# Performance work log

Measured on AMD Instinct MI355X. Metric: run time of the kernel, lower is better.

The kernel has to match this reference:

```python
import jax, jax.numpy as jnp
import numpy as np

N_HEADS = 8
D_MODEL = 128
EPS = 1e-6


def setup_inputs() -> dict:
    key = jax.random.key(0)
    k1, k2, k3, k4, k5 = jax.random.split(key, 5)
    B, Dim, F, T = 1, D_MODEL, 256, 1024
    queries = jax.random.normal(k1, (B, Dim, F, T), dtype=jnp.float32)
    keys = jax.random.normal(k2, (B, Dim, F, T), dtype=jnp.float32)
    values = jax.random.normal(k3, (B, Dim, F, T), dtype=jnp.float32)
    # out_projection: Linear(d_model, d_output) with d_output == d_model
    W_out = jax.random.normal(k4, (D_MODEL, D_MODEL), dtype=jnp.float32) / np.sqrt(D_MODEL)
    b_out = jax.random.normal(k5, (D_MODEL,), dtype=jnp.float32) * 0.01
    return {"queries": queries, "keys": keys, "values": values,
            "W_out": W_out, "b_out": b_out}


def _to_heads(x, B, Dim, L, H):
    # (B, Dim, F, T) -> (B, L, Dim) -> (B, L, H, d) -> (B, H, L, d)
    return x.reshape(B, Dim, L).transpose(0, 2, 1).reshape(B, L, H, Dim // H).transpose(0, 2, 1, 3)


def reference(queries, keys, values, W_out, b_out):
    B, Dim, F, T = queries.shape
    L = F * T
    H = N_HEADS
    q = jax.nn.sigmoid(_to_heads(queries, B, Dim, L, H))  # (B,H,L,d)
    k = jax.nn.sigmoid(_to_heads(keys, B, Dim, L, H))
    v = _to_heads(values, B, Dim, L, H)

    # NOTE: sums are over the HEAD axis (dim=1), faithful to the original code
    ks = k.sum(axis=1, keepdims=True)                      # (B,1,L,d)
    qs = q.sum(axis=1, keepdims=True)
    sink_incoming = 1.0 / jnp.sum((q + EPS) * (ks + EPS), axis=-1)      # (B,H,L)
    source_outgoing = 1.0 / jnp.sum((k + EPS) * (qs + EPS), axis=-1)    # (B,H,L)
    conserved_sink = jnp.sum(
        (q + EPS) * ((k * source_outgoing[..., None]).sum(axis=1, keepdims=True) + EPS),
        axis=-1)                                                        # (B,H,L)
    conserved_source = jnp.sum(
        (k + EPS) * ((q * sink_incoming[..., None]).sum(axis=1, keepdims=True) + EPS),
        axis=-1)
    conserved_source = jnp.clip(conserved_source, -1.0, 1.0)
    sink_allocation = jax.nn.sigmoid(conserved_sink * (float(L) / float(L)))
    source_competition = jax.nn.softmax(conserved_source, axis=-1) * float(L)

    kv = jnp.einsum('bhld,bhlm->bhdm', k, v * source_competition[..., None])
    qkv = jnp.einsum('bhld,bhdm->bhlm', q * sink_incoming[..., None], kv)
    x = (qkv * sink_allocation[..., None]).transpose(0, 2, 1, 3).reshape(B, L, Dim)
    x = x @ W_out.T + b_out                                 # dropout is identity (eval)
    return x.transpose(0, 2, 1).reshape(B, Dim, F, T)
```

## Files before the change

kernel.cpp:

```cpp
#include <hip/hip_runtime.h>
#include <hip/hip_bf16.h>

#define L_TOT (1 << 18)
#define L_SHIFT 18
#define NHEAD 8
#define DHEAD 16
#define DMODEL 128
#define EPSF 1e-6f

typedef float f32x4 __attribute__((ext_vector_type(4)));
typedef short bf16x8 __attribute__((ext_vector_type(8)));

__device__ __forceinline__ float frcp(float x) { return __builtin_amdgcn_rcpf(x); }
__device__ __forceinline__ float sigm(float x) { return frcp(1.0f + __expf(-x)); }
__device__ __forceinline__ unsigned short f2bf(float f) {
    return (unsigned short)((__float_as_uint(f) + 0x8000u) >> 16);
}

__device__ __forceinline__ float qsum(float x) {
    x += __int_as_float(__builtin_amdgcn_update_dpp(0, __float_as_int(x), 0xB1, 0xf, 0xf, true));
    x += __int_as_float(__builtin_amdgcn_update_dpp(0, __float_as_int(x), 0x4E, 0xf, 0xf, true));
    return x;
}

__global__ __launch_bounds__(256) void k1_stats(
        const float* __restrict__ Q, const float* __restrict__ K,
        float* __restrict__ scale_o, float* __restrict__ wbuf,
        float* __restrict__ sep) {
    __shared__ float hredl[4][8];

    const int t = threadIdx.x;
    const int l0 = blockIdx.x * 64;
    const int c = t >> 2;
    const int s = t & 3;
    const int l = l0 + c;

    float qv[32], kv[32];
#pragma unroll
    for (int h = 0; h < 8; ++h)
#pragma unroll
        for (int r = 0; r < 4; ++r) {
            const int p = h * 16 + s * 4 + r;
            qv[h * 4 + r] = Q[(p << L_SHIFT) + l];
            kv[h * 4 + r] = K[(p << L_SHIFT) + l];
        }

    unsigned a[32];
#pragma unroll
    for (int i = 0; i < 32; ++i) {
        const unsigned qu = __float_as_uint(sigm(qv[i])) + 0x8000u;
        const unsigned ku = __float_as_uint(sigm(kv[i])) + 0x8000u;
        a[i] = __builtin_amdgcn_perm(ku, qu, 0x07060302u);
    }

    float ks[4] = {0.f, 0.f, 0.f, 0.f}, qs[4] = {0.f, 0.f, 0.f, 0.f};
#pragma unroll
    for (int h = 0; h < 8; ++h)
#pragma unroll
        for (int j = 0; j < 4; ++j) {
            const unsigned u = a[h * 4 + j];
            qs[j] += __uint_as_float(u << 16);
            ks[j] += __uint_as_float(u & 0xffff0000u);
        }

    float kse[4], qse[4];
#pragma unroll
    for (int j = 0; j < 4; ++j) { kse[j] = ks[j] + EPSF; qse[j] = qs[j] + EPSF; }

    float si[8], so[8];
#pragma unroll
    for (int h = 0; h < 8; ++h) {
        float aq = 0.f, ak = 0.f;
#pragma unroll
        for (int j = 0; j < 4; ++j) {
            const unsigned u = a[h * 4 + j];
            aq += __uint_as_float(u << 16) * kse[j];
            ak += __uint_as_float(u & 0xffff0000u) * qse[j];
        }
        si[h] = frcp(qsum(aq));
        so[h] = frcp(qsum(ak));
    }

    float kso[4] = {0.f, 0.f, 0.f, 0.f}, qsi[4] = {0.f, 0.f, 0.f, 0.f};
#pragma unroll
    for (int h = 0; h < 8; ++h)
#pragma unroll
        for (int j = 0; j < 4; ++j) {
            const unsigned u = a[h * 4 + j];
            kso[j] += __uint_as_float(u & 0xffff0000u) * so[h];
            qsi[j] += __uint_as_float(u << 16) * si[h];
        }
#pragma unroll
    for (int j = 0; j < 4; ++j) { kse[j] = kso[j] + EPSF; qse[j] = qsi[j] + EPSF; }

    float e2[2], sc2[2];
#pragma unroll
    for (int h = 0; h < 8; ++h) {
        float aq = 0.f, ak = 0.f;
#pragma unroll
        for (int j = 0; j < 4; ++j) {
            const unsigned u = a[h * 4 + j];
            aq += __uint_as_float(u << 16) * kse[j];
            ak += __uint_as_float(u & 0xffff0000u) * qse[j];
        }
        const float ck = qsum(aq);
        float cs = qsum(ak);
        if ((h >> 1) == s) {
            cs = fminf(fmaxf(cs, -1.f), 1.f);
            e2[h & 1] = __expf(cs);
            sc2[h & 1] = sigm(ck) * si[h];
        }
    }

    wbuf[((2 * s + 0) << L_SHIFT) + l] = e2[0];
    wbuf[((2 * s + 1) << L_SHIFT) + l] = e2[1];
    scale_o[((2 * s + 0) << L_SHIFT) + l] = sc2[0];
    scale_o[((2 * s + 1) << L_SHIFT) + l] = sc2[1];

    float v0 = e2[0], v1 = e2[1];
    v0 += __shfl_xor(v0, 4, 64);  v1 += __shfl_xor(v1, 4, 64);
    v0 += __shfl_xor(v0, 8, 64);  v1 += __shfl_xor(v1, 8, 64);
    v0 += __shfl_xor(v0, 16, 64); v1 += __shfl_xor(v1, 16, 64);
    v0 += __shfl_xor(v0, 32, 64); v1 += __shfl_xor(v1, 32, 64);
    if ((t & 63) < 4) {
        const int w = t >> 6;
        hredl[w][2 * s + 0] = v0;
        hredl[w][2 * s + 1] = v1;
    }
    __syncthreads();
    if (t < 8)
        sep[blockIdx.x * 8 + t] = hredl[0][t] + hredl[1][t] + hredl[2][t] + hredl[3][t];
}

__global__ __launch_bounds__(256) void k2_kv(
        const float* __restrict__ Kg, const float* __restrict__ Vg,
        const float* __restrict__ wg, float* __restrict__ parts) {
    __shared__ float kvred[4][256];
    const int b = blockIdx.x;
    const int h = b >> 7;
    const int blk = b & 127;
    const int t = threadIdx.x;
    const int wv = t >> 6, lane = t & 63;
    const int lq = lane & 15, lh = lane >> 4;

    const int rowKV = ((h * DHEAD + lq) << L_SHIFT);
    const int rowW  = (h << L_SHIFT);
    const int lbase = blk * 2048 + wv * 512 + lh * 8;

    f32x4 acc = {0.f, 0.f, 0.f, 0.f};
#pragma unroll 4
    for (int ch = 0; ch < 16; ++ch) {
        const int lo = lbase + ch * 32;
        const float4 ka = *(const float4*)&Kg[rowKV + lo];
        const float4 kb = *(const float4*)&Kg[rowKV + lo + 4];
        const float4 va = *(const float4*)&Vg[rowKV + lo];
        const float4 vb = *(const float4*)&Vg[rowKV + lo + 4];
        const float4 wa = *(const float4*)&wg[rowW + lo];
        const float4 wb = *(const float4*)&wg[rowW + lo + 4];
        bf16x8 af, bvf;
        af[0] = (short)f2bf(sigm(ka.x) * wa.x);
        af[1] = (short)f2bf(sigm(ka.y) * wa.y);
        af[2] = (short)f2bf(sigm(ka.z) * wa.z);
        af[3] = (short)f2bf(sigm(ka.w) * wa.w);
        af[4] = (short)f2bf(sigm(kb.x) * wb.x);
        af[5] = (short)f2bf(sigm(kb.y) * wb.y);
        af[6] = (short)f2bf(sigm(kb.z) * wb.z);
        af[7] = (short)f2bf(sigm(kb.w) * wb.w);
        bvf[0] = (short)f2bf(va.x);
        bvf[1] = (short)f2bf(va.y);
        bvf[2] = (short)f2bf(va.z);
        bvf[3] = (short)f2bf(va.w);
        bvf[4] = (short)f2bf(vb.x);
        bvf[5] = (short)f2bf(vb.y);
        bvf[6] = (short)f2bf(vb.z);
        bvf[7] = (short)f2bf(vb.w);
        acc = __builtin_amdgcn_mfma_f32_16x16x32_bf16(af, bvf, acc, 0, 0, 0);
    }

#pragma unroll
    for (int r = 0; r < 4; ++r)
        kvred[wv][(lh * 4 + r) * 16 + lq] = acc[r];
    __syncthreads();
    parts[b * 256 + t] = kvred[0][t] + kvred[1][t] + kvred[2][t] + kvred[3][t];
}

__global__ __launch_bounds__(256) void k3_wkv(
        const float* __restrict__ Wg, const float* __restrict__ parts,
        const float* __restrict__ sep, unsigned* __restrict__ wkvb) {
    const int hb = blockIdx.x;
    const int t = threadIdx.x;
    __shared__ float kvf[256];
    __shared__ float redl[4];

    float p = 0.f;
#pragma unroll
    for (int i = 0; i < 16; ++i) p += sep[(t + i * 256) * 8 + hb];
#pragma unroll
    for (int o = 32; o >= 1; o >>= 1) p += __shfl_xor(p, o, 64);
    if ((t & 63) == 0) redl[t >> 6] = p;

    float kacc = 0.f;
    for (int j = 0; j < 128; ++j)
        kacc += parts[(hb * 128 + j) * 256 + t];

    __syncthreads();
    const float s = (float)L_TOT / (redl[0] + redl[1] + redl[2] + redl[3]);
    kvf[t] = kacc * s;
    __syncthreads();

#pragma unroll
    for (int i = 0; i < 4; ++i) {
        const int j = t + i * 256;
        const int dim = j & 127, prp = j >> 7;
        float a0 = 0.f, a1 = 0.f;
#pragma unroll
        for (int mm = 0; mm < 16; ++mm) {
            const float wv = Wg[dim * 128 + hb * 16 + mm];
            a0 += wv * kvf[(2 * prp) * 16 + mm];
            a1 += wv * kvf[(2 * prp + 1) * 16 + mm];
        }
        wkvb[dim * 64 + hb * 8 + prp] = ((unsigned)f2bf(a1) << 16) | f2bf(a0);
    }
}

__global__ __launch_bounds__(256) void k4_mfma(
        const float* __restrict__ Q, const float* __restrict__ scale_g,
        const unsigned* __restrict__ wkvb, const float* __restrict__ bg,
        float* __restrict__ out) {
    __shared__ unsigned A_lds[128 * 68];
    __shared__ float bias[128];
    const int t = threadIdx.x;

#pragma unroll
    for (int i = 0; i < 8; ++i) {
        const int idx4 = t + i * 256;
        const uint4 v = ((const uint4*)wkvb)[idx4];
        const int row = idx4 >> 4, c4 = idx4 & 15;
        *(uint4*)&A_lds[row * 68 + c4 * 4] = v;
    }
    if (t < 128) bias[t] = bg[t];
    __syncthreads();

    const int w = t >> 6, lane = t & 63;
    const int lq = lane & 15, lh = lane >> 4;

#pragma unroll
    for (int ci = 0; ci < 2; ++ci) {
        const int l = blockIdx.x * 128 + ci * 64 + w * 16 + lq;

        float qv[4][8];
        float scv[4];
#pragma unroll
        for (int ks = 0; ks < 4; ++ks) {
            scv[ks] = scale_g[((ks * 2 + (lane >> 5)) << L_SHIFT) + l];
#pragma unroll
            for (int j = 0; j < 8; ++j) {
                const int p = ks * 32 + lh * 8 + j;
                qv[ks][j] = Q[(p << L_SHIFT) + l];
            }
        }
        bf16x8 bfr[4];
#pragma unroll
        for (int ks = 0; ks < 4; ++ks)
#pragma unroll
            for (int j = 0; j < 8; ++j)
                bfr[ks][j] = (short)f2bf(sigm(qv[ks][j]) * scv[ks]);

        f32x4 acc[8];
#pragma unroll
        for (int mt = 0; mt < 8; ++mt)
            acc[mt] = *(const f32x4*)&bias[mt * 16 + lh * 4];

#pragma unroll
        for (int ks = 0; ks < 4; ++ks) {
#pragma unroll
            for (int mt = 0; mt < 8; ++mt) {
                const int row = mt * 16 + lq;
                const bf16x8 aA = *(const bf16x8*)&A_lds[row * 68 + ks * 16 + lh * 4];
                acc[mt] = __builtin_amdgcn_mfma_f32_16x16x32_bf16(aA, bfr[ks], acc[mt], 0, 0, 0);
            }
        }

#pragma unroll
        for (int mt = 0; mt < 8; ++mt) {
#pragma unroll
            for (int r = 0; r < 4; ++r) {
                const int dim = mt * 16 + lh * 4 + r;
                out[(dim << L_SHIFT) + l] = acc[mt][r];
            }
        }
    }
}

extern "C" void kernel_launch(void* const* d_in, const int* in_sizes, int n_in,
                              void* d_out, int out_size, void* d_ws, size_t ws_size,
                              hipStream_t stream) {
    const float* Q = (const float*)d_in[0];
    const float* K = (const float*)d_in[1];
    const float* V = (const float*)d_in[2];
    const float* W = (const float*)d_in[3];
    const float* B = (const float*)d_in[4];
    float* out = (float*)d_out;
    float* ws = (float*)d_ws;

    float* parts    = ws;
    unsigned* wkvb  = (unsigned*)(ws + 262144);
    float* sep      = ws + 270336;
    float* scale    = ws + 303104;
    float* wbuf     = scale + 8 * L_TOT;

    k1_stats<<<L_TOT / 64, 256, 0, stream>>>(Q, K, scale, wbuf, sep);
    k2_kv<<<NHEAD * 128, 256, 0, stream>>>(K, V, wbuf, parts);
    k3_wkv<<<NHEAD, 256, 0, stream>>>(W, parts, sep, wkvb);
    k4_mfma<<<L_TOT / 128, 256, 0, stream>>>(Q, scale, wkvb, B, out);
}
```

Baseline: 190.6 us.

## Process four column groups per k1 block with software-pipelined loads

k1_stats now handles 256 positions per block instead of 64, looping over four 64-column chunks. The next chunk's Q/K loads are issued before the current chunk's stats are computed, so memory latency overlaps with compute. Per-block exp partial sums are accumulated across chunks, so the sep buffer shrinks and k3's reduction loop over it is cut to match. The cost is higher register pressure (two 32-element load buffers plus the packed array) and a quarter as many blocks, which may reduce occupancy and latency hiding.

```diff
diff --git a/kernel.cpp b/kernel.cpp
--- a/kernel.cpp
+++ b/kernel.cpp
@@ -23,36 +23,32 @@
     return x;
 }
 
-__global__ __launch_bounds__(256) void k1_stats(
+__device__ __forceinline__ void k1_load(
         const float* __restrict__ Q, const float* __restrict__ K,
-        float* __restrict__ scale_o, float* __restrict__ wbuf,
-        float* __restrict__ sep) {
-    __shared__ float hredl[4][8];
-
-    const int t = threadIdx.x;
-    const int l0 = blockIdx.x * 64;
-    const int c = t >> 2;
-    const int s = t & 3;
-    const int l = l0 + c;
-
-    float qv[32], kv[32];
+        int l, int s, float* qv, float* kvv) {
 #pragma unroll
     for (int h = 0; h < 8; ++h)
 #pragma unroll
         for (int r = 0; r < 4; ++r) {
             const int p = h * 16 + s * 4 + r;
-            qv[h * 4 + r] = Q[(p << L_SHIFT) + l];
-            kv[h * 4 + r] = K[(p << L_SHIFT) + l];
-        }
-
-    unsigned a[32];
+            qv[h * 4 + r]  = Q[(p << L_SHIFT) + l];
+            kvv[h * 4 + r] = K[(p << L_SHIFT) + l];
+        }
+}
+
+__device__ __forceinline__ void k1_pack(const float* qv, const float* kvv, unsigned* a) {
 #pragma unroll
     for (int i = 0; i < 32; ++i) {
         const unsigned qu = __float_as_uint(sigm(qv[i])) + 0x8000u;
-        const unsigned ku = __float_as_uint(sigm(kv[i])) + 0x8000u;
+        const unsigned ku = __float_as_uint(sigm(kvv[i])) + 0x8000u;
         a[i] = __builtin_amdgcn_perm(ku, qu, 0x07060302u);
     }
-
+}
+
+__device__ __forceinline__ void k1_body(
+        const unsigned* a, int l, int s,
+        float* __restrict__ scale_o, float* __restrict__ wbuf,
+        float& acc0, float& acc1) {
     float ks[4] = {0.f, 0.f, 0.f, 0.f}, qs[4] = {0.f, 0.f, 0.f, 0.f};
 #pragma unroll
     for (int h = 0; h < 8; ++h)
@@ -117,7 +113,40 @@
     scale_o[((2 * s + 0) << L_SHIFT) + l] = sc2[0];
     scale_o[((2 * s + 1) << L_SHIFT) + l] = sc2[1];
 
-    float v0 = e2[0], v1 = e2[1];
+    acc0 += e2[0];
+    acc1 += e2[1];
+}
+
+__global__ __launch_bounds__(256) void k1_stats(
+        const float* __restrict__ Q, const float* __restrict__ K,
+        float* __restrict__ scale_o, float* __restrict__ wbuf,
+        float* __restrict__ sep) {
+    __shared__ float hredl[4][8];
+
+    const int t = threadIdx.x;
+    const int s = t & 3;
+    const int cq = t >> 2;
+    const int lb = blockIdx.x * 256 + cq;
+
+    float qv[32], kvv[32];
+    unsigned a[32];
+    float acc0 = 0.f, acc1 = 0.f;
+
+    k1_load(Q, K, lb, s, qv, kvv);
+
+    k1_pack(qv, kvv, a);
+    k1_load(Q, K, lb + 64, s, qv, kvv);
+    k1_body(a, lb, s, scale_o, wbuf, acc0, acc1);
+    k1_pack(qv, kvv, a);
+    k1_load(Q, K, lb + 128, s, qv, kvv);
+    k1_body(a, lb + 64, s, scale_o, wbuf, acc0, acc1);
+    k1_pack(qv, kvv, a);
+    k1_load(Q, K, lb + 192, s, qv, kvv);
+    k1_body(a, lb + 128, s, scale_o, wbuf, acc0, acc1);
+    k1_pack(qv, kvv, a);
+    k1_body(a, lb + 192, s, scale_o, wbuf, acc0, acc1);
+
+    float v0 = acc0, v1 = acc1;
     v0 += __shfl_xor(v0, 4, 64);  v1 += __shfl_xor(v1, 4, 64);
     v0 += __shfl_xor(v0, 8, 64);  v1 += __shfl_xor(v1, 8, 64);
     v0 += __shfl_xor(v0, 16, 64); v1 += __shfl_xor(v1, 16, 64);
@@ -194,7 +223,7 @@
 
     float p = 0.f;
 #pragma unroll
-    for (int i = 0; i < 16; ++i) p += sep[(t + i * 256) * 8 + hb];
+    for (int i = 0; i < 4; ++i) p += sep[(t + i * 256) * 8 + hb];
 #pragma unroll
     for (int o = 32; o >= 1; o >>= 1) p += __shfl_xor(p, o, 64);
     if ((t & 63) == 0) redl[t >> 6] = p;
@@ -309,7 +338,7 @@
     float* scale    = ws + 303104;
     float* wbuf     = scale + 8 * L_TOT;
 
-    k1_stats<<<L_TOT / 64, 256, 0, stream>>>(Q, K, scale, wbuf, sep);
+    k1_stats<<<L_TOT / 256, 256, 0, stream>>>(Q, K, scale, wbuf, sep);
     k2_kv<<<NHEAD * 128, 256, 0, stream>>>(K, V, wbuf, parts);
     k3_wkv<<<NHEAD, 256, 0, stream>>>(W, parts, sep, wkvb);
     k4_mfma<<<L_TOT / 128, 256, 0, stream>>>(Q, scale, wkvb, B, out);
```

Result: slower. 200.5 us (+5.2%).

## Fuse stats and KV-accumulation kernels so sigmoid weights stay in LDS

Applied to the files above, without the earlier changes.

Merges the per-position stats kernel and the K^T·V MFMA accumulation kernel into one kernel. Each block processes 256 positions in four chunks. The softmax numerators are kept in shared memory instead of being written to and re-read from a global buffer, and K is re-read right after the stats pass, while it is likely still cached. This removes one full global read of K and the write and read of the weight buffer. In exchange there are fewer, heavier blocks and per-block partials grow eightfold, so the single-wave-per-head reduction kernel now loops over 1024 partials and could become latency-bound.

```diff
diff --git a/kernel.cpp b/kernel.cpp
--- a/kernel.cpp
+++ b/kernel.cpp
@@ -23,165 +23,183 @@
     return x;
 }
 
-__global__ __launch_bounds__(256) void k1_stats(
+__device__ __forceinline__ f32x4 kv_mfma(const float* __restrict__ Kp,
+                                         const float* __restrict__ Vp,
+                                         float4 wa, float4 wb, f32x4 acc) {
+    const float4 ka = *(const float4*)Kp;
+    const float4 kb = *(const float4*)(Kp + 4);
+    const float4 va = *(const float4*)Vp;
+    const float4 vb = *(const float4*)(Vp + 4);
+    bf16x8 af, bvf;
+    af[0] = (short)f2bf(sigm(ka.x) * wa.x);
+    af[1] = (short)f2bf(sigm(ka.y) * wa.y);
+    af[2] = (short)f2bf(sigm(ka.z) * wa.z);
+    af[3] = (short)f2bf(sigm(ka.w) * wa.w);
+    af[4] = (short)f2bf(sigm(kb.x) * wb.x);
+    af[5] = (short)f2bf(sigm(kb.y) * wb.y);
+    af[6] = (short)f2bf(sigm(kb.z) * wb.z);
+    af[7] = (short)f2bf(sigm(kb.w) * wb.w);
+    bvf[0] = (short)f2bf(va.x);
+    bvf[1] = (short)f2bf(va.y);
+    bvf[2] = (short)f2bf(va.z);
+    bvf[3] = (short)f2bf(va.w);
+    bvf[4] = (short)f2bf(vb.x);
+    bvf[5] = (short)f2bf(vb.y);
+    bvf[6] = (short)f2bf(vb.z);
+    bvf[7] = (short)f2bf(vb.w);
+    return __builtin_amdgcn_mfma_f32_16x16x32_bf16(af, bvf, acc, 0, 0, 0);
+}
+
+__global__ __launch_bounds__(256) void k12_fused(
         const float* __restrict__ Q, const float* __restrict__ K,
-        float* __restrict__ scale_o, float* __restrict__ wbuf,
-        float* __restrict__ sep) {
+        const float* __restrict__ V,
+        float* __restrict__ scale_o, float* __restrict__ sep,
+        float* __restrict__ parts) {
+    __shared__ float wlds[8][64];
     __shared__ float hredl[4][8];
 
     const int t = threadIdx.x;
-    const int l0 = blockIdx.x * 64;
+    const int b = blockIdx.x;
     const int c = t >> 2;
     const int s = t & 3;
-    const int l = l0 + c;
-
-    float qv[32], kv[32];
-#pragma unroll
-    for (int h = 0; h < 8; ++h)
-#pragma unroll
-        for (int r = 0; r < 4; ++r) {
-            const int p = h * 16 + s * 4 + r;
-            qv[h * 4 + r] = Q[(p << L_SHIFT) + l];
-            kv[h * 4 + r] = K[(p << L_SHIFT) + l];
-        }
-
-    unsigned a[32];
-#pragma unroll
-    for (int i = 0; i < 32; ++i) {
-        const unsigned qu = __float_as_uint(sigm(qv[i])) + 0x8000u;
-        const unsigned ku = __float_as_uint(sigm(kv[i])) + 0x8000u;
-        a[i] = __builtin_amdgcn_perm(ku, qu, 0x07060302u);
-    }
-
-    float ks[4] = {0.f, 0.f, 0.f, 0.f}, qs[4] = {0.f, 0.f, 0.f, 0.f};
-#pragma unroll
-    for (int h = 0; h < 8; ++h)
-#pragma unroll
-        for (int j = 0; j < 4; ++j) {
-            const unsigned u = a[h * 4 + j];
-            qs[j] += __uint_as_float(u << 16);
-            ks[j] += __uint_as_float(u & 0xffff0000u);
-        }
-
-    float kse[4], qse[4];
-#pragma unroll
-    for (int j = 0; j < 4; ++j) { kse[j] = ks[j] + EPSF; qse[j] = qs[j] + EPSF; }
-
-    float si[8], so[8];
-#pragma unroll
-    for (int h = 0; h < 8; ++h) {
-        float aq = 0.f, ak = 0.f;
-#pragma unroll
-        for (int j = 0; j < 4; ++j) {
-            const unsigned u = a[h * 4 + j];
-            aq += __uint_as_float(u << 16) * kse[j];
-            ak += __uint_as_float(u & 0xffff0000u) * qse[j];
-        }
-        si[h] = frcp(qsum(aq));
-        so[h] = frcp(qsum(ak));
-    }
-
-    float kso[4] = {0.f, 0.f, 0.f, 0.f}, qsi[4] = {0.f, 0.f, 0.f, 0.f};
-#pragma unroll
-    for (int h = 0; h < 8; ++h)
-#pragma unroll
-        for (int j = 0; j < 4; ++j) {
-            const unsigned u = a[h * 4 + j];
-            kso[j] += __uint_as_float(u & 0xffff0000u) * so[h];
-            qsi[j] += __uint_as_float(u << 16) * si[h];
-        }
-#pragma unroll
-    for (int j = 0; j < 4; ++j) { kse[j] = kso[j] + EPSF; qse[j] = qsi[j] + EPSF; }
-
-    float e2[2], sc2[2];
-#pragma unroll
-    for (int h = 0; h < 8; ++h) {
-        float aq = 0.f, ak = 0.f;
-#pragma unroll
-        for (int j = 0; j < 4; ++j) {
-            const unsigned u = a[h * 4 + j];
-            aq += __uint_as_float(u << 16) * kse[j];
-            ak += __uint_as_float(u & 0xffff0000u) * qse[j];
-        }
-        const float ck = qsum(aq);
-        float cs = qsum(ak);
-        if ((h >> 1) == s) {
-            cs = fminf(fmaxf(cs, -1.f), 1.f);
-            e2[h & 1] = __expf(cs);
-            sc2[h & 1] = sigm(ck) * si[h];
-        }
-    }
-
-    wbuf[((2 * s + 0) << L_SHIFT) + l] = e2[0];
-    wbuf[((2 * s + 1) << L_SHIFT) + l] = e2[1];
-    scale_o[((2 * s + 0) << L_SHIFT) + l] = sc2[0];
-    scale_o[((2 * s + 1) << L_SHIFT) + l] = sc2[1];
-
-    float v0 = e2[0], v1 = e2[1];
+    const int lane = t & 63;
+    const int wv = t >> 6;
+    const int lq = lane & 15, lh = lane >> 4;
+    const int h0 = 2 * wv, h1 = 2 * wv + 1;
+
+    float accse0 = 0.f, accse1 = 0.f;
+    f32x4 acc0 = {0.f, 0.f, 0.f, 0.f};
+    f32x4 acc1 = {0.f, 0.f, 0.f, 0.f};
+
+    for (int ch = 0; ch < 4; ++ch) {
+        const int l0 = b * 256 + ch * 64;
+        const int l = l0 + c;
+
+        float qv[32], kvv[32];
+#pragma unroll
+        for (int h = 0; h < 8; ++h)
+#pragma unroll
+            for (int r = 0; r < 4; ++r) {
+                const int p = h * 16 + s * 4 + r;
+                qv[h * 4 + r]  = Q[(p << L_SHIFT) + l];
+                kvv[h * 4 + r] = K[(p << L_SHIFT) + l];
+            }
+
+        unsigned a[32];
+#pragma unroll
+        for (int i = 0; i < 32; ++i) {
+            const unsigned qu = __float_as_uint(sigm(qv[i])) + 0x8000u;
+            const unsigned ku = __float_as_uint(sigm(kvv[i])) + 0x8000u;
+            a[i] = __builtin_amdgcn_perm(ku, qu, 0x07060302u);
+        }
+
+        float ks[4] = {0.f, 0.f, 0.f, 0.f}, qs[4] = {0.f, 0.f, 0.f, 0.f};
+#pragma unroll
+        for (int h = 0; h < 8; ++h)
+#pragma unroll
+            for (int j = 0; j < 4; ++j) {
+                const unsigned u = a[h * 4 + j];
+                qs[j] += __uint_as_float(u << 16);
+                ks[j] += __uint_as_float(u & 0xffff0000u);
+            }
+
+        float kse[4], qse[4];
+#pragma unroll
+        for (int j = 0; j < 4; ++j) { kse[j] = ks[j] + EPSF; qse[j] = qs[j] + EPSF; }
+
+        float si[8], so[8];
+#pragma unroll
+        for (int h = 0; h < 8; ++h) {
+            float aq = 0.f, ak = 0.f;
+#pragma unroll
+            for (int j = 0; j < 4; ++j) {
+                const unsigned u = a[h * 4 + j];
+                aq += __uint_as_float(u << 16) * kse[j];
+                ak += __uint_as_float(u & 0xffff0000u) * qse[j];
+            }
+            si[h] = frcp(qsum(aq));
+            so[h] = frcp(qsum(ak));
+        }
+
+        float kso[4] = {0.f, 0.f, 0.f, 0.f}, qsi[4] = {0.f, 0.f, 0.f, 0.f};
+#pragma unroll
+        for (int h = 0; h < 8; ++h)
+#pragma unroll
+            for (int j = 0; j < 4; ++j) {
+                const unsigned u = a[h * 4 + j];
+                kso[j] += __uint_as_float(u & 0xffff0000u) * so[h];
+                qsi[j] += __uint_as_float(u << 16) * si[h];
+            }
+#pragma unroll
+        for (int j = 0; j < 4; ++j) { kse[j] = kso[j] + EPSF; qse[j] = qsi[j] + EPSF; }
+
+        float e2[2], sc2[2];
+#pragma unroll
+        for (int h = 0; h < 8; ++h) {
+            float aq = 0.f, ak = 0.f;
+#pragma unroll
+            for (int j = 0; j < 4; ++j) {
+                const unsigned u = a[h * 4 + j];
+                aq += __uint_as_float(u << 16) * kse[j];
+                ak += __uint_as_float(u & 0xffff0000u) * qse[j];
+            }
+            const float ck = qsum(aq);
+            float cs = qsum(ak);
+            if ((h >> 1) == s) {
+                cs = fminf(fmaxf(cs, -1.f), 1.f);
+                e2[h & 1] = __expf(cs);
+                sc2[h & 1] = sigm(ck) * si[h];
+            }
+        }
+
+        scale_o[((2 * s + 0) << L_SHIFT) + l] = sc2[0];
+        scale_o[((2 * s + 1) << L_SHIFT) + l] = sc2[1];
+        wlds[2 * s + 0][c] = e2[0];
+        wlds[2 * s + 1][c] = e2[1];
+        accse0 += e2[0];
+        accse1 += e2[1];
+        __syncthreads();
+
+#pragma unroll
+        for (int ksr = 0; ksr < 2; ++ksr) {
+            const int lo = l0 + ksr * 32 + lh * 8;
+            const int wo = ksr * 32 + lh * 8;
+            {
+                const float4 wa = *(const float4*)&wlds[h0][wo];
+                const float4 wb = *(const float4*)&wlds[h0][wo + 4];
+                acc0 = kv_mfma(&K[((h0 * DHEAD + lq) << L_SHIFT) + lo],
+                               &V[((h0 * DHEAD + lq) << L_SHIFT) + lo],
+                               wa, wb, acc0);
+            }
+            {
+                const float4 wa = *(const float4*)&wlds[h1][wo];
+                const float4 wb = *(const float4*)&wlds[h1][wo + 4];
+                acc1 = kv_mfma(&K[((h1 * DHEAD + lq) << L_SHIFT) + lo],
+                               &V[((h1 * DHEAD + lq) << L_SHIFT) + lo],
+                               wa, wb, acc1);
+            }
+        }
+        __syncthreads();
+    }
+
+#pragma unroll
+    for (int r = 0; r < 4; ++r) {
+        parts[((b * 8 + h0) << 8) + (lh * 4 + r) * 16 + lq] = acc0[r];
+        parts[((b * 8 + h1) << 8) + (lh * 4 + r) * 16 + lq] = acc1[r];
+    }
+
+    float v0 = accse0, v1 = accse1;
     v0 += __shfl_xor(v0, 4, 64);  v1 += __shfl_xor(v1, 4, 64);
     v0 += __shfl_xor(v0, 8, 64);  v1 += __shfl_xor(v1, 8, 64);
     v0 += __shfl_xor(v0, 16, 64); v1 += __shfl_xor(v1, 16, 64);
     v0 += __shfl_xor(v0, 32, 64); v1 += __shfl_xor(v1, 32, 64);
     if ((t & 63) < 4) {
-        const int w = t >> 6;
-        hredl[w][2 * s + 0] = v0;
-        hredl[w][2 * s + 1] = v1;
+        hredl[wv][2 * s + 0] = v0;
+        hredl[wv][2 * s + 1] = v1;
     }
     __syncthreads();
     if (t < 8)
-        sep[blockIdx.x * 8 + t] = hredl[0][t] + hredl[1][t] + hredl[2][t] + hredl[3][t];
-}
-
-__global__ __launch_bounds__(256) void k2_kv(
-        const float* __restrict__ Kg, const float* __restrict__ Vg,
-        const float* __restrict__ wg, float* __restrict__ parts) {
-    __shared__ float kvred[4][256];
-    const int b = blockIdx.x;
-    const int h = b >> 7;
-    const int blk = b & 127;
-    const int t = threadIdx.x;
-    const int wv = t >> 6, lane = t & 63;
-    const int lq = lane & 15, lh = lane >> 4;
-
-    const int rowKV = ((h * DHEAD + lq) << L_SHIFT);
-    const int rowW  = (h << L_SHIFT);
-    const int lbase = blk * 2048 + wv * 512 + lh * 8;
-
-    f32x4 acc = {0.f, 0.f, 0.f, 0.f};
-#pragma unroll 4
-    for (int ch = 0; ch < 16; ++ch) {
-        const int lo = lbase + ch * 32;
-        const float4 ka = *(const float4*)&Kg[rowKV + lo];
-        const float4 kb = *(const float4*)&Kg[rowKV + lo + 4];
-        const float4 va = *(const float4*)&Vg[rowKV + lo];
-        const float4 vb = *(const float4*)&Vg[rowKV + lo + 4];
-        const float4 wa = *(const float4*)&wg[rowW + lo];
-        const float4 wb = *(const float4*)&wg[rowW + lo + 4];
-        bf16x8 af, bvf;
-        af[0] = (short)f2bf(sigm(ka.x) * wa.x);
-        af[1] = (short)f2bf(sigm(ka.y) * wa.y);
-        af[2] = (short)f2bf(sigm(ka.z) * wa.z);
-        af[3] = (short)f2bf(sigm(ka.w) * wa.w);
-        af[4] = (short)f2bf(sigm(kb.x) * wb.x);
-        af[5] = (short)f2bf(sigm(kb.y) * wb.y);
-        af[6] = (short)f2bf(sigm(kb.z) * wb.z);
-        af[7] = (short)f2bf(sigm(kb.w) * wb.w);
-        bvf[0] = (short)f2bf(va.x);
-        bvf[1] = (short)f2bf(va.y);
-        bvf[2] = (short)f2bf(va.z);
-        bvf[3] = (short)f2bf(va.w);
-        bvf[4] = (short)f2bf(vb.x);
-        bvf[5] = (short)f2bf(vb.y);
-        bvf[6] = (short)f2bf(vb.z);
-        bvf[7] = (short)f2bf(vb.w);
-        acc = __builtin_amdgcn_mfma_f32_16x16x32_bf16(af, bvf, acc, 0, 0, 0);
-    }
-
-#pragma unroll
-    for (int r = 0; r < 4; ++r)
-        kvred[wv][(lh * 4 + r) * 16 + lq] = acc[r];
-    __syncthreads();
-    parts[b * 256 + t] = kvred[0][t] + kvred[1][t] + kvred[2][t] + kvred[3][t];
+        sep[b * 8 + t] = hredl[0][t] + hredl[1][t] + hredl[2][t] + hredl[3][t];
 }
 
 __global__ __launch_bounds__(256) void k3_wkv(
@@ -194,14 +212,19 @@
 
     float p = 0.f;
 #pragma unroll
-    for (int i = 0; i < 16; ++i) p += sep[(t + i * 256) * 8 + hb];
+    for (int i = 0; i < 4; ++i) p += sep[(t + i * 256) * 8 + hb];
 #pragma unroll
     for (int o = 32; o >= 1; o >>= 1) p += __shfl_xor(p, o, 64);
     if ((t & 63) == 0) redl[t >> 6] = p;
 
-    float kacc = 0.f;
-    for (int j = 0; j < 128; ++j)
-        kacc += parts[(hb * 128 + j) * 256 + t];
+    float ka0 = 0.f, ka1 = 0.f, ka2 = 0.f, ka3 = 0.f;
+    for (int j = 0; j < 1024; j += 4) {
+        ka0 += parts[(((j + 0) * 8 + hb) << 8) + t];
+        ka1 += parts[(((j + 1) * 8 + hb) << 8) + t];
+        ka2 += parts[(((j + 2) * 8 + hb) << 8) + t];
+        ka3 += parts[(((j + 3) * 8 + hb) << 8) + t];
+    }
+    const float kacc = (ka0 + ka1) + (ka2 + ka3);
 
     __syncthreads();
     const float s = (float)L_TOT / (redl[0] + redl[1] + redl[2] + redl[3]);
@@ -304,13 +327,11 @@
     float* ws = (float*)d_ws;
 
     float* parts    = ws;
-    unsigned* wkvb  = (unsigned*)(ws + 262144);
-    float* sep      = ws + 270336;
-    float* scale    = ws + 303104;
-    float* wbuf     = scale + 8 * L_TOT;
-
-    k1_stats<<<L_TOT / 64, 256, 0, stream>>>(Q, K, scale, wbuf, sep);
-    k2_kv<<<NHEAD * 128, 256, 0, stream>>>(K, V, wbuf, parts);
+    unsigned* wkvb  = (unsigned*)(ws + 2097152);
+    float* sep      = ws + 2105344;
+    float* scale    = ws + 2113536;
+
+    k12_fused<<<1024, 256, 0, stream>>>(Q, K, V, scale, sep, parts);
     k3_wkv<<<NHEAD, 256, 0, stream>>>(W, parts, sep, wkvb);
     k4_mfma<<<L_TOT / 128, 256, 0, stream>>>(Q, scale, wkvb, B, out);
 }
```

Measured after the change: 217.4 us. +14.1%, slower.
